# Performance work log

Measured on AMD Instinct MI355X. Metric: run time of the kernel, lower is better.

## Reference

```python
import jax, jax.numpy as jnp
import numpy as np


def _gcn_layer(h, src, dst, W, b, norm_src, norm_dst, n_nodes):
    # DGL GraphConv with norm='both': D_out^{-1/2} -> sum-aggregate -> D_in^{-1/2} -> XW + b
    m = (h * norm_src[:, None])[src]                       # [E, d] gather
    agg = jax.ops.segment_sum(m, dst, num_segments=n_nodes)  # [N, d] scatter-add
    return agg * norm_dst[:, None] @ W + b


def reference(features, src, dst, W1, b1, W2, b2):
    n_nodes = features.shape[0]
    ones = jnp.ones(src.shape[0], dtype=features.dtype)
    deg_out = jax.ops.segment_sum(ones, src, num_segments=n_nodes)
    deg_in = jax.ops.segment_sum(ones, dst, num_segments=n_nodes)
    # DGL clamps degrees to min 1 before the -1/2 power
    norm_src = jnp.clip(deg_out, 1.0, None) ** -0.5
    norm_dst = jnp.clip(deg_in, 1.0, None) ** -0.5

    h = jax.nn.relu(_gcn_layer(features, src, dst, W1, b1, norm_src, norm_dst, n_nodes))
    h = jax.nn.relu(_gcn_layer(h, src, dst, W2, b2, norm_src, norm_dst, n_nodes))
    return h


def setup_inputs() -> dict:
    key = jax.random.key(0)
    k1, k2, k3, k4, k5 = jax.random.split(key, 5)
    N, E, D = 50000, 600000, 128
    scale = 1.0 / np.sqrt(D)
    return {
        "features": jax.random.normal(k1, (N, D), dtype=jnp.float32),
        "src": jax.random.randint(k2, (E,), 0, N, dtype=jnp.int32),
        "dst": jax.random.randint(k3, (E,), 0, N, dtype=jnp.int32),
        "W1": jax.random.normal(k4, (D, D), dtype=jnp.float32) * scale,
        "b1": jnp.zeros((D,), dtype=jnp.float32),
        "W2": jax.random.normal(k5, (D, D), dtype=jnp.float32) * scale,
        "b2": jnp.zeros((D,), dtype=jnp.float32),
    }
```

## Files before the change

kernel.cpp:

```cpp
#include <hip/hip_runtime.h>

#define DIM 128
#define HBD 64
#define HBS 64
#define HWORDS 25088
#define WSTR 136

typedef __attribute__((ext_vector_type(8))) short b8;
typedef __attribute__((ext_vector_type(4))) float f4;
typedef __attribute__((ext_vector_type(8))) unsigned short u16x8;

static __device__ __forceinline__ unsigned short f2bf(float f) {
    unsigned u = __float_as_uint(f);
    u += 0x7fffu + ((u >> 16) & 1u);
    return (unsigned short)(u >> 16);
}
static __device__ __forceinline__ float bf2f(unsigned short b) {
    return __uint_as_float((unsigned)b << 16);
}

__global__ __launch_bounds__(1024) void k_hist(const int* __restrict__ src,
                                               const int* __restrict__ dst,
                                               unsigned short* __restrict__ local,
                                               unsigned* __restrict__ hist_in,
                                               unsigned* __restrict__ hist_out,
                                               int E, int W2p, int slice_d, int slice_s) {
    __shared__ unsigned h[HWORDS];
    const int t = threadIdx.x;
    const bool is_dst = blockIdx.x < HBD;
    const int b = is_dst ? blockIdx.x : blockIdx.x - HBD;
    const int slice = is_dst ? slice_d : slice_s;
    const int e0 = b * slice;
    const int e1 = min(e0 + slice, E);
    const int W4 = W2p >> 2;
    uint4* h4 = (uint4*)h;

    for (int w = t; w < W4; w += 1024) h4[w] = make_uint4(0u, 0u, 0u, 0u);
    __syncthreads();

    if (is_dst) {
        int e = e0 + t;
        int d = (e < e1) ? dst[e] : 0;
        while (e < e1) {
            int en = e + 1024;
            int dn = (en < e1) ? dst[en] : 0;
            unsigned sh = (unsigned)(d & 1) * 16u;
            unsigned old = atomicAdd(&h[d >> 1], 1u << sh);
            local[e] = (unsigned short)((old >> sh) & 0xffffu);
            e = en; d = dn;
        }
    } else {
        int e = e0 + t;
        int s = (e < e1) ? src[e] : 0;
        while (e < e1) {
            int en = e + 1024;
            int sn = (en < e1) ? src[en] : 0;
            atomicAdd(&h[s >> 1], 1u << ((unsigned)(s & 1) * 16u));
            e = en; s = sn;
        }
    }
    __syncthreads();

    uint4* o = (uint4*)((is_dst ? hist_in : hist_out) + (size_t)b * W2p);
    for (int w = t; w < W4; w += 1024) o[w] = h4[w];
}

__global__ __launch_bounds__(256) void k_colscan(unsigned* __restrict__ hist_in,
                                                 const unsigned* __restrict__ hist_out,
                                                 int* __restrict__ cnt,
                                                 int* __restrict__ deg_out,
                                                 int* __restrict__ bsum,
                                                 int W2, int W2p, int N) {
    __shared__ int wsum[4];
    int w = blockIdx.x * 256 + threadIdx.x;
    unsigned run = 0;
    if (w < W2) {
        unsigned* p = hist_in + w;
        #pragma unroll 8
        for (int b = 0; b < HBD; ++b) {
            unsigned x = *p;
            *p = run;
            run += x;
            p += W2p;
        }
        unsigned run2 = 0;
        const unsigned* q = hist_out + w;
        #pragma unroll 8
        for (int b = 0; b < HBS; ++b) { run2 += *q; q += W2p; }
        int n0 = w * 2;
        if (n0 + 1 < N) {
            *(int2*)(cnt + n0)     = make_int2((int)(run & 0xffffu), (int)(run >> 16));
            *(int2*)(deg_out + n0) = make_int2((int)(run2 & 0xffffu), (int)(run2 >> 16));
        } else {
            cnt[n0]     = (int)(run & 0xffffu);
            deg_out[n0] = (int)(run2 & 0xffffu);
            run &= 0xffffu;
        }
    }
    int tot = (int)(run & 0xffffu) + (int)(run >> 16);
    #pragma unroll
    for (int off = 32; off > 0; off >>= 1) tot += __shfl_down(tot, off, 64);
    int lane = threadIdx.x & 63, wave = threadIdx.x >> 6;
    if (lane == 0) wsum[wave] = tot;
    __syncthreads();
    if (threadIdx.x == 0)   bsum[2 * blockIdx.x]     = wsum[0] + wsum[1];
    if (threadIdx.x == 128) bsum[2 * blockIdx.x + 1] = wsum[2] + wsum[3];
}

__global__ __launch_bounds__(256) void k_edge_pass_fb(const int* __restrict__ src,
                                                      const int* __restrict__ dst,
                                                      int* __restrict__ deg_out,
                                                      int* __restrict__ cnt,
                                                      int* __restrict__ local_fb, int E) {
    int e = blockIdx.x * 256 + threadIdx.x;
    if (e < E) {
        atomicAdd(&deg_out[src[e]], 1);
        local_fb[e] = atomicAdd(&cnt[dst[e]], 1);
    }
}

__global__ __launch_bounds__(256) void k_block_reduce(const int* __restrict__ deg,
                                                      int* __restrict__ bsum, int N) {
    __shared__ int wsum[4];
    int i = blockIdx.x * 256 + threadIdx.x;
    int x = (i < N) ? deg[i] : 0;
    #pragma unroll
    for (int off = 32; off > 0; off >>= 1) x += __shfl_down(x, off, 64);
    int lane = threadIdx.x & 63, wave = threadIdx.x >> 6;
    if (lane == 0) wsum[wave] = x;
    __syncthreads();
    if (threadIdx.x == 0) bsum[blockIdx.x] = wsum[0] + wsum[1] + wsum[2] + wsum[3];
}

__global__ __launch_bounds__(256) void k_scan_final(const int* __restrict__ cnt,
                                                    const int* __restrict__ deg_out,
                                                    const int* __restrict__ bsum,
                                                    int* __restrict__ row_off,
                                                    float* __restrict__ norm_src,
                                                    float* __restrict__ norm_dst, int N) {
    __shared__ int wsum[4];
    __shared__ int base_s;
    const int t = threadIdx.x;
    const int lane = t & 63, wave = t >> 6;

    int pre = 0;
    for (int i = t; i < blockIdx.x; i += 256) pre += bsum[i];
    #pragma unroll
    for (int off = 32; off > 0; off >>= 1) pre += __shfl_down(pre, off, 64);
    if (lane == 0) wsum[wave] = pre;
    __syncthreads();
    if (t == 0) base_s = wsum[0] + wsum[1] + wsum[2] + wsum[3];
    __syncthreads();
    const int bpre_v = base_s;

    int i = blockIdx.x * 256 + t;
    int x = (i < N) ? cnt[i] : 0;
    int orig = x;
    #pragma unroll
    for (int off = 1; off < 64; off <<= 1) {
        int y = __shfl_up(x, off, 64);
        if (lane >= off) x += y;
    }
    if (lane == 63) wsum[wave] = x;
    __syncthreads();
    if (t == 0) {
        int s = 0;
        for (int w = 0; w < 4; ++w) { int tt = wsum[w]; wsum[w] = s; s += tt; }
    }
    __syncthreads();
    x += wsum[wave] + bpre_v;
    if (i < N) {
        row_off[i] = x - orig;
        int di = orig < 1 ? 1 : orig;
        norm_dst[i] = rsqrtf((float)di);
        int dov = deg_out[i]; if (dov < 1) dov = 1;
        norm_src[i] = rsqrtf((float)dov);
    }
    if (i == N - 1) row_off[N] = x;
}

__global__ __launch_bounds__(256) void k_fill_cast_prep(
        const int* __restrict__ src, const int* __restrict__ dst,
        const int* __restrict__ row_off,
        const unsigned short* __restrict__ local,
        const int* __restrict__ local_fb,
        const unsigned* __restrict__ hist_in,
        int* __restrict__ csr_src,
        const float* __restrict__ feat, const float* __restrict__ norm_src,
        unsigned short* __restrict__ fbf,
        const float* __restrict__ W1, const float* __restrict__ W2,
        unsigned short* __restrict__ w1hi, unsigned short* __restrict__ w1lo,
        unsigned short* __restrict__ w2hi, unsigned short* __restrict__ w2lo,
        int E, int W2p, int slice, int eb, int cb, int pb, int n4) {
    int bx = blockIdx.x;
    if (bx < eb) {
        int e = bx * 256 + threadIdx.x;
        if (e < E) {
            int d = dst[e];
            int pos = row_off[d];
            if (hist_in) {
                int b = e / slice;
                unsigned sh = (unsigned)(d & 1) * 16u;
                unsigned bo = (hist_in[(size_t)b * W2p + (d >> 1)] >> sh) & 0xffffu;
                pos += (int)bo + (int)local[e];
            } else {
                pos += local_fb[e];
            }
            csr_src[pos] = src[e];
        }
    } else if (bx < eb + cb) {
        int i = (bx - eb) * 256 + threadIdx.x;
        if (i < n4) {
            float4 v = ((const float4*)feat)[i];
            float ns = norm_src[i >> 5];
            ushort4 o;
            o.x = f2bf(v.x * ns); o.y = f2bf(v.y * ns);
            o.z = f2bf(v.z * ns); o.w = f2bf(v.w * ns);
            ((ushort4*)fbf)[i] = o;
        }
    } else {
        int b = bx - eb - cb;
        const float* W; unsigned short *Hi, *Lo;
        if (b < pb) { W = W1; Hi = w1hi; Lo = w1lo; } else { W = W2; Hi = w2hi; Lo = w2lo; b -= pb; }
        int e = b * 256 + threadIdx.x;
        if (e < DIM * DIM) {
            int k = e >> 7, c = e & 127;
            float w = W[e];
            unsigned short hi = f2bf(w);
            unsigned short lo = f2bf(w - bf2f(hi));
            Hi[c * DIM + k] = hi;
            Lo[c * DIM + k] = lo;
        }
    }
}

__global__ __launch_bounds__(256) void k_spmm(const unsigned short* __restrict__ hb,
                                              const int* __restrict__ csr_src,
                                              const int* __restrict__ row_off,
                                              const float* __restrict__ norm_dst,
                                              unsigned short* __restrict__ aggbf, int N) {
    int t = blockIdx.x * 256 + threadIdx.x;
    int node = t >> 4;
    int lane = t & 15;
    if (node >= N) return;
    int beg = row_off[node], end = row_off[node + 1];
    float a0[8] = {0.f, 0.f, 0.f, 0.f, 0.f, 0.f, 0.f, 0.f};
    float a1[8] = {0.f, 0.f, 0.f, 0.f, 0.f, 0.f, 0.f, 0.f};
    int i = beg;
    for (; i + 4 <= end; i += 4) {
        int s0 = csr_src[i], s1 = csr_src[i + 1], s2 = csr_src[i + 2], s3 = csr_src[i + 3];
        u16x8 u0 = *((const u16x8*)(hb + (size_t)s0 * DIM) + lane);
        u16x8 u1 = *((const u16x8*)(hb + (size_t)s1 * DIM) + lane);
        u16x8 u2 = *((const u16x8*)(hb + (size_t)s2 * DIM) + lane);
        u16x8 u3 = *((const u16x8*)(hb + (size_t)s3 * DIM) + lane);
        #pragma unroll
        for (int j = 0; j < 8; ++j) {
            a0[j] += bf2f(u0[j]);
            a1[j] += bf2f(u1[j]);
            a0[j] += bf2f(u2[j]);
            a1[j] += bf2f(u3[j]);
        }
    }
    for (; i < end; ++i) {
        int s0 = csr_src[i];
        u16x8 u0 = *((const u16x8*)(hb + (size_t)s0 * DIM) + lane);
        #pragma unroll
        for (int j = 0; j < 8; ++j) a0[j] += bf2f(u0[j]);
    }
    float nd = norm_dst[node];
    u16x8 o;
    #pragma unroll
    for (int j = 0; j < 8; ++j) o[j] = f2bf((a0[j] + a1[j]) * nd);
    *((u16x8*)(aggbf + (size_t)node * DIM) + lane) = o;
}

__global__ __launch_bounds__(256, 2) void k_gemm_mfma(
        const unsigned short* __restrict__ A,
        const unsigned short* __restrict__ Wt_hi,
        const unsigned short* __restrict__ Wt_lo,
        const float* __restrict__ bias,
        const float* __restrict__ postscale,
        float* __restrict__ outf, unsigned short* __restrict__ outbf, int N) {
    __shared__ unsigned short WH[DIM * WSTR];
    __shared__ unsigned short WL[DIM * WSTR];

    const int t = threadIdx.x;
    #pragma unroll
    for (int i = 0; i < 8; ++i) {
        int e = (t + i * 256) * 8;
        int c = e >> 7, k = e & 127;
        *(float4*)(WH + c * WSTR + k) = *(const float4*)(Wt_hi + e);
        *(float4*)(WL + c * WSTR + k) = *(const float4*)(Wt_lo + e);
    }
    __syncthreads();

    const int wv = t >> 6;
    const int l = t & 63;
    const int m = l & 15;
    const int quad = l >> 4;
    const int row_t0 = blockIdx.x * 128 + wv * 32;

    f4 acc[2][8];
    #pragma unroll
    for (int rt = 0; rt < 2; ++rt)
        #pragma unroll
        for (int ct = 0; ct < 8; ++ct)
            acc[rt][ct] = (f4){0.f, 0.f, 0.f, 0.f};

    int r0 = row_t0 + m;      if (r0 >= N) r0 = N - 1;
    int r1 = row_t0 + 16 + m; if (r1 >= N) r1 = N - 1;

    #pragma unroll
    for (int ks = 0; ks < 4; ++ks) {
        int koff = ks * 32 + quad * 8;
        b8 a0 = *(const b8*)(A + (size_t)r0 * DIM + koff);
        b8 a1 = *(const b8*)(A + (size_t)r1 * DIM + koff);
        #pragma unroll
        for (int ct = 0; ct < 8; ++ct) {
            int c = ct * 16 + m;
            b8 bh = *(const b8*)(WH + c * WSTR + koff);
            b8 bl = *(const b8*)(WL + c * WSTR + koff);
            acc[0][ct] = __builtin_amdgcn_mfma_f32_16x16x32_bf16(a0, bh, acc[0][ct], 0, 0, 0);
            acc[0][ct] = __builtin_amdgcn_mfma_f32_16x16x32_bf16(a0, bl, acc[0][ct], 0, 0, 0);
            acc[1][ct] = __builtin_amdgcn_mfma_f32_16x16x32_bf16(a1, bh, acc[1][ct], 0, 0, 0);
            acc[1][ct] = __builtin_amdgcn_mfma_f32_16x16x32_bf16(a1, bl, acc[1][ct], 0, 0, 0);
        }
    }

    #pragma unroll
    for (int rt = 0; rt < 2; ++rt) {
        int rowb = row_t0 + rt * 16 + quad * 4;
        #pragma unroll
        for (int r = 0; r < 4; ++r) {
            int gr = rowb + r;
            if (gr < N) {
                float s = postscale ? postscale[gr] : 1.f;
                #pragma unroll
                for (int ct = 0; ct < 8; ++ct) {
                    int col = ct * 16 + m;
                    float v = fmaxf(acc[rt][ct][r] + bias[col], 0.f) * s;
                    if (outbf) outbf[(size_t)gr * DIM + col] = f2bf(v);
                    else       outf[(size_t)gr * DIM + col] = v;
                }
            }
        }
    }
}

static inline size_t align_up(size_t x, size_t a) { return (x + a - 1) & ~(a - 1); }

extern "C" void kernel_launch(void* const* d_in, const int* in_sizes, int n_in,
                              void* d_out, int out_size, void* d_ws, size_t ws_size,
                              hipStream_t stream) {
    const float* features = (const float*)d_in[0];
    const int*   src      = (const int*)d_in[1];
    const int*   dst      = (const int*)d_in[2];
    const float* W1       = (const float*)d_in[3];
    const float* b1       = (const float*)d_in[4];
    const float* W2       = (const float*)d_in[5];
    const float* b2       = (const float*)d_in[6];
    float* out = (float*)d_out;

    const int N = in_sizes[0] / DIM;
    const int E = in_sizes[1];
    const int B = (N + 255) / 256;
    const int W2w = (N + 1) >> 1;
    const int W2p = (W2w + 3) & ~3;
    const int slice_d = (E + HBD - 1) / HBD;
    const int slice_s = (E + HBS - 1) / HBS;
    const int cs_blocks = (W2w + 255) / 256;

    size_t nodeb = align_up((size_t)N * 4, 256);
    char* p = (char*)d_ws;
    int*   deg_out  = (int*)p;                      p += nodeb;
    int*   cnt      = (int*)p;                      p += nodeb;
    float* norm_src = (float*)p;                    p += nodeb;
    float* norm_dst = (float*)p;                    p += nodeb;
    int*   row_off  = (int*)p;                      p += align_up((size_t)(N + 1) * 4, 256);
    int*   bsum     = (int*)p;                      p += align_up((size_t)(2 * cs_blocks) * 4, 256);
    int*   csr_src  = (int*)p;                      p += align_up((size_t)E * 4, 256);
    char*  big      = p;                            p += 2 * (size_t)N * DIM * 4;
    unsigned short* w1hi = (unsigned short*)p;      p += (size_t)DIM * DIM * 2;
    unsigned short* w1lo = (unsigned short*)p;      p += (size_t)DIM * DIM * 2;
    unsigned short* w2hi = (unsigned short*)p;      p += (size_t)DIM * DIM * 2;
    unsigned short* w2lo = (unsigned short*)p;      p += (size_t)DIM * DIM * 2;
    unsigned short* aggbf = (unsigned short*)big;
    unsigned short* h1bf  = (unsigned short*)(big + (size_t)N * DIM * 2);
    unsigned short* fbf   = (unsigned short*)(big + 3 * (size_t)N * DIM * 2);
    char* ap = big;
    unsigned short* local = (unsigned short*)ap;    ap += align_up((size_t)E * 2, 256);
    unsigned* hist_in  = (unsigned*)ap;             ap += (size_t)HBD * W2p * 4;
    unsigned* hist_out = (unsigned*)ap;             ap += (size_t)HBS * W2p * 4;
    int* local_fb = (int*)big;

    const int edge_blocks = (E + 255) / 256;
    const int spmm_blocks = (int)(((size_t)N * 16 + 255) / 256);
    const int gemm_blocks = (N + 127) / 128;
    const int n4 = N * (DIM / 4);
    const int cast_blocks = (n4 + 255) / 256;
    const int prep_blocks = (DIM * DIM + 255) / 256;
    const int fcp_blocks  = edge_blocks + cast_blocks + 2 * prep_blocks;

    const bool fast = (W2p <= HWORDS) &&
        (align_up((size_t)E * 2, 256) + (size_t)(HBD + HBS) * W2p * 4
            <= 3 * (size_t)N * DIM * 2);

    if (fast) {
        k_hist<<<HBD + HBS, 1024, 0, stream>>>(src, dst, local, hist_in, hist_out,
                                               E, W2p, slice_d, slice_s);
        k_colscan<<<cs_blocks, 256, 0, stream>>>(hist_in, hist_out, cnt, deg_out, bsum, W2w, W2p, N);
        k_scan_final<<<B, 256, 0, stream>>>(cnt, deg_out, bsum, row_off, norm_src, norm_dst, N);
        k_fill_cast_prep<<<fcp_blocks, 256, 0, stream>>>(
            src, dst, row_off, local, (const int*)nullptr, hist_in, csr_src,
            features, norm_src, fbf, W1, W2, w1hi, w1lo, w2hi, w2lo,
            E, W2p, slice_d, edge_blocks, cast_blocks, prep_blocks, n4);
    } else {
        hipMemsetAsync(deg_out, 0, nodeb * 2, stream);
        k_edge_pass_fb<<<edge_blocks, 256, 0, stream>>>(src, dst, deg_out, cnt, local_fb, E);
        k_block_reduce<<<B, 256, 0, stream>>>(cnt, bsum, N);
        k_scan_final<<<B, 256, 0, stream>>>(cnt, deg_out, bsum, row_off, norm_src, norm_dst, N);
        k_fill_cast_prep<<<fcp_blocks, 256, 0, stream>>>(
            src, dst, row_off, (const unsigned short*)nullptr, local_fb,
            (const unsigned*)nullptr, csr_src,
            features, norm_src, fbf, W1, W2, w1hi, w1lo, w2hi, w2lo,
            E, W2p, slice_d, edge_blocks, cast_blocks, prep_blocks, n4);
    }

    k_spmm<<<spmm_blocks, 256, 0, stream>>>(fbf, csr_src, row_off, norm_dst, aggbf, N);
    k_gemm_mfma<<<gemm_blocks, 256, 0, stream>>>(aggbf, w1hi, w1lo, b1, norm_src,
                                                 (float*)nullptr, h1bf, N);

    k_spmm<<<spmm_blocks, 256, 0, stream>>>(h1bf, csr_src, row_off, norm_dst, aggbf, N);
    k_gemm_mfma<<<gemm_blocks, 256, 0, stream>>>(aggbf, w2hi, w2lo, b2, (const float*)nullptr,
                                                 out, (unsigned short*)nullptr, N);
}
```

Baseline: 207.4 us.

## Fuse preprocessing launches and move source normalization into SpMM gather

```diff
diff --git a/kernel.cpp b/kernel.cpp
--- a/kernel.cpp
+++ b/kernel.cpp
@@ -24,87 +24,183 @@
                                                unsigned short* __restrict__ local,
                                                unsigned* __restrict__ hist_in,
                                                unsigned* __restrict__ hist_out,
-                                               int E, int W2p, int slice_d, int slice_s) {
-    __shared__ unsigned h[HWORDS];
+                                               const float* __restrict__ feat,
+                                               unsigned short* __restrict__ fbf,
+                                               const float* __restrict__ W1,
+                                               const float* __restrict__ W2,
+                                               unsigned short* __restrict__ w1hi,
+                                               unsigned short* __restrict__ w1lo,
+                                               unsigned short* __restrict__ w2hi,
+                                               unsigned short* __restrict__ w2lo,
+                                               int* __restrict__ scan_aux,
+                                               int E, int W2p, int slice_d, int slice_s,
+                                               int n4) {
     const int t = threadIdx.x;
-    const bool is_dst = blockIdx.x < HBD;
-    const int b = is_dst ? blockIdx.x : blockIdx.x - HBD;
-    const int slice = is_dst ? slice_d : slice_s;
-    const int e0 = b * slice;
-    const int e1 = min(e0 + slice, E);
-    const int W4 = W2p >> 2;
-    uint4* h4 = (uint4*)h;
-
-    for (int w = t; w < W4; w += 1024) h4[w] = make_uint4(0u, 0u, 0u, 0u);
-    __syncthreads();
-
-    if (is_dst) {
-        int e = e0 + t;
-        int d = (e < e1) ? dst[e] : 0;
-        while (e < e1) {
-            int en = e + 1024;
-            int dn = (en < e1) ? dst[en] : 0;
-            unsigned sh = (unsigned)(d & 1) * 16u;
-            unsigned old = atomicAdd(&h[d >> 1], 1u << sh);
-            local[e] = (unsigned short)((old >> sh) & 0xffffu);
-            e = en; d = dn;
+    const int bx = blockIdx.x;
+    if (bx < HBD + HBS) {
+        __shared__ unsigned h[HWORDS];
+        const bool is_dst = bx < HBD;
+        const int b = is_dst ? bx : bx - HBD;
+        const int slice = is_dst ? slice_d : slice_s;
+        const int e0 = b * slice;
+        const int e1 = min(e0 + slice, E);
+        const int W4 = W2p >> 2;
+        uint4* h4 = (uint4*)h;
+
+        for (int w = t; w < W4; w += 1024) h4[w] = make_uint4(0u, 0u, 0u, 0u);
+        __syncthreads();
+
+        if (is_dst) {
+            int e = e0 + t;
+            int d = (e < e1) ? dst[e] : 0;
+            while (e < e1) {
+                int en = e + 1024;
+                int dn = (en < e1) ? dst[en] : 0;
+                unsigned sh = (unsigned)(d & 1) * 16u;
+                unsigned old = atomicAdd(&h[d >> 1], 1u << sh);
+                local[e] = (unsigned short)((old >> sh) & 0xffffu);
+                e = en; d = dn;
+            }
+        } else {
+            int e = e0 + t;
+            int s = (e < e1) ? src[e] : 0;
+            while (e < e1) {
+                int en = e + 1024;
+                int sn = (en < e1) ? src[en] : 0;
+                atomicAdd(&h[s >> 1], 1u << ((unsigned)(s & 1) * 16u));
+                e = en; s = sn;
+            }
+        }
+        __syncthreads();
+
+        uint4* o = (uint4*)((is_dst ? hist_in : hist_out) + (size_t)b * W2p);
+        for (int w = t; w < W4; w += 1024) o[w] = h4[w];
+    } else if (bx < HBD + HBS + 2) {
+        int b = bx - (HBD + HBS);
+        if (b == 0 && t < 256) scan_aux[t] = 0;
+        const float* W = b ? W2 : W1;
+        unsigned short* Hi = b ? w2hi : w1hi;
+        unsigned short* Lo = b ? w2lo : w1lo;
+        for (int e = t; e < DIM * DIM; e += 1024) {
+            int k = e >> 7, c = e & 127;
+            float w = W[e];
+            unsigned short hi = f2bf(w);
+            unsigned short lo = f2bf(w - bf2f(hi));
+            Hi[c * DIM + k] = hi;
+            Lo[c * DIM + k] = lo;
         }
     } else {
-        int e = e0 + t;
-        int s = (e < e1) ? src[e] : 0;
-        while (e < e1) {
-            int en = e + 1024;
-            int sn = (en < e1) ? src[en] : 0;
-            atomicAdd(&h[s >> 1], 1u << ((unsigned)(s & 1) * 16u));
-            e = en; s = sn;
-        }
-    }
-    __syncthreads();
-
-    uint4* o = (uint4*)((is_dst ? hist_in : hist_out) + (size_t)b * W2p);
-    for (int w = t; w < W4; w += 1024) o[w] = h4[w];
-}
-
-__global__ __launch_bounds__(256) void k_colscan(unsigned* __restrict__ hist_in,
-                                                 const unsigned* __restrict__ hist_out,
-                                                 int* __restrict__ cnt,
-                                                 int* __restrict__ deg_out,
-                                                 int* __restrict__ bsum,
-                                                 int W2, int W2p, int N) {
+        int i = (bx - (HBD + HBS + 2)) * 1024 + t;
+        if (i < n4) {
+            float4 v = ((const float4*)feat)[i];
+            ushort4 o;
+            o.x = f2bf(v.x); o.y = f2bf(v.y);
+            o.z = f2bf(v.z); o.w = f2bf(v.w);
+            ((ushort4*)fbf)[i] = o;
+        }
+    }
+}
+
+__global__ __launch_bounds__(256) void k_scan(unsigned* __restrict__ hist_in,
+                                              const unsigned* __restrict__ hist_out,
+                                              int* __restrict__ partials,
+                                              int* __restrict__ flags,
+                                              int* __restrict__ row_off,
+                                              float* __restrict__ norm_src,
+                                              float* __restrict__ norm_dst,
+                                              int W2, int W2p, int N) {
     __shared__ int wsum[4];
-    int w = blockIdx.x * 256 + threadIdx.x;
-    unsigned run = 0;
+    __shared__ int wbase[4];
+    __shared__ int psum[4];
+    __shared__ int base_s;
+    const int t = threadIdx.x;
+    const int b = blockIdx.x;
+    const int w = b * 256 + t;
+    const int lane = t & 63, wave = t >> 6;
+
+    unsigned run = 0, run2 = 0;
     if (w < W2) {
         unsigned* p = hist_in + w;
         #pragma unroll 8
-        for (int b = 0; b < HBD; ++b) {
+        for (int i = 0; i < HBD; ++i) {
             unsigned x = *p;
             *p = run;
             run += x;
             p += W2p;
         }
-        unsigned run2 = 0;
         const unsigned* q = hist_out + w;
         #pragma unroll 8
-        for (int b = 0; b < HBS; ++b) { run2 += *q; q += W2p; }
-        int n0 = w * 2;
-        if (n0 + 1 < N) {
-            *(int2*)(cnt + n0)     = make_int2((int)(run & 0xffffu), (int)(run >> 16));
-            *(int2*)(deg_out + n0) = make_int2((int)(run2 & 0xffffu), (int)(run2 >> 16));
-        } else {
-            cnt[n0]     = (int)(run & 0xffffu);
-            deg_out[n0] = (int)(run2 & 0xffffu);
-            run &= 0xffffu;
-        }
-    }
-    int tot = (int)(run & 0xffffu) + (int)(run >> 16);
-    #pragma unroll
-    for (int off = 32; off > 0; off >>= 1) tot += __shfl_down(tot, off, 64);
-    int lane = threadIdx.x & 63, wave = threadIdx.x >> 6;
-    if (lane == 0) wsum[wave] = tot;
-    __syncthreads();
-    if (threadIdx.x == 0)   bsum[2 * blockIdx.x]     = wsum[0] + wsum[1];
-    if (threadIdx.x == 128) bsum[2 * blockIdx.x + 1] = wsum[2] + wsum[3];
+        for (int i = 0; i < HBS; ++i) { run2 += *q; q += W2p; }
+    }
+    const int n0 = w * 2, n1 = n0 + 1;
+    const int lo = (int)(run & 0xffffu), hi = (int)(run >> 16);
+    const int s = (w < W2) ? (lo + ((n1 < N) ? hi : 0)) : 0;
+
+    int x = s;
+    #pragma unroll
+    for (int off = 1; off < 64; off <<= 1) {
+        int y = __shfl_up(x, off, 64);
+        if (lane >= off) x += y;
+    }
+    if (lane == 63) wsum[wave] = x;
+    __syncthreads();
+    if (t == 0) {
+        int acc = 0;
+        #pragma unroll
+        for (int i = 0; i < 4; ++i) { int v = wsum[i]; wbase[i] = acc; acc += v; }
+        partials[b] = acc;
+        __threadfence();
+        atomicExch(&flags[b], 1);
+    }
+    __syncthreads();
+
+    int pre = 0;
+    if (t < b) {
+        while (atomicAdd(&flags[t], 0) == 0) { __builtin_amdgcn_s_sleep(2); }
+        pre = atomicAdd(&partials[t], 0);
+    }
+    #pragma unroll
+    for (int off = 32; off > 0; off >>= 1) pre += __shfl_down(pre, off, 64);
+    if (lane == 0) psum[wave] = pre;
+    __syncthreads();
+    if (t == 0) base_s = psum[0] + psum[1] + psum[2] + psum[3];
+    __syncthreads();
+    const int B = base_s;
+
+    if (w < W2) {
+        int tb = B + wbase[wave] + (x - s);
+        row_off[n0] = tb;
+        int dlo = lo < 1 ? 1 : lo;
+        norm_dst[n0] = rsqrtf((float)dlo);
+        int o0 = (int)(run2 & 0xffffu); if (o0 < 1) o0 = 1;
+        norm_src[n0] = rsqrtf((float)o0);
+        if (n1 < N) {
+            row_off[n1] = tb + lo;
+            int dhi = hi < 1 ? 1 : hi;
+            norm_dst[n1] = rsqrtf((float)dhi);
+            int o1 = (int)(run2 >> 16); if (o1 < 1) o1 = 1;
+            norm_src[n1] = rsqrtf((float)o1);
+            if (n1 == N - 1) row_off[N] = tb + lo + hi;
+        } else if (n0 == N - 1) {
+            row_off[N] = tb + lo;
+        }
+    }
+}
+
+__global__ __launch_bounds__(256) void k_fill(const int* __restrict__ src,
+                                              const int* __restrict__ dst,
+                                              const int* __restrict__ row_off,
+                                              const unsigned short* __restrict__ local,
+                                              const unsigned* __restrict__ hist_in,
+                                              int* __restrict__ csr_src,
+                                              int E, int W2p, int slice) {
+    int e = blockIdx.x * 256 + threadIdx.x;
+    if (e >= E) return;
+    int d = dst[e];
+    int b = e / slice;
+    unsigned sh = (unsigned)(d & 1) * 16u;
+    unsigned bo = (hist_in[(size_t)b * W2p + (d >> 1)] >> sh) & 0xffffu;
+    csr_src[row_off[d] + (int)bo + (int)local[e]] = src[e];
 }
 
 __global__ __launch_bounds__(256) void k_edge_pass_fb(const int* __restrict__ src,
@@ -179,43 +275,31 @@
     if (i == N - 1) row_off[N] = x;
 }
 
-__global__ __launch_bounds__(256) void k_fill_cast_prep(
+__global__ __launch_bounds__(256) void k_fill_cast_prep_fb(
         const int* __restrict__ src, const int* __restrict__ dst,
         const int* __restrict__ row_off,
-        const unsigned short* __restrict__ local,
         const int* __restrict__ local_fb,
-        const unsigned* __restrict__ hist_in,
         int* __restrict__ csr_src,
-        const float* __restrict__ feat, const float* __restrict__ norm_src,
+        const float* __restrict__ feat,
         unsigned short* __restrict__ fbf,
         const float* __restrict__ W1, const float* __restrict__ W2,
         unsigned short* __restrict__ w1hi, unsigned short* __restrict__ w1lo,
         unsigned short* __restrict__ w2hi, unsigned short* __restrict__ w2lo,
-        int E, int W2p, int slice, int eb, int cb, int pb, int n4) {
+        int E, int eb, int cb, int pb, int n4) {
     int bx = blockIdx.x;
     if (bx < eb) {
         int e = bx * 256 + threadIdx.x;
         if (e < E) {
             int d = dst[e];
-            int pos = row_off[d];
-            if (hist_in) {
-                int b = e / slice;
-                unsigned sh = (unsigned)(d & 1) * 16u;
-                unsigned bo = (hist_in[(size_t)b * W2p + (d >> 1)] >> sh) & 0xffffu;
-                pos += (int)bo + (int)local[e];
-            } else {
-                pos += local_fb[e];
-            }
-            csr_src[pos] = src[e];
+            csr_src[row_off[d] + local_fb[e]] = src[e];
         }
     } else if (bx < eb + cb) {
         int i = (bx - eb) * 256 + threadIdx.x;
         if (i < n4) {
             float4 v = ((const float4*)feat)[i];
-            float ns = norm_src[i >> 5];
             ushort4 o;
-            o.x = f2bf(v.x * ns); o.y = f2bf(v.y * ns);
-            o.z = f2bf(v.z * ns); o.w = f2bf(v.w * ns);
+            o.x = f2bf(v.x); o.y = f2bf(v.y);
+            o.z = f2bf(v.z); o.w = f2bf(v.w);
             ((ushort4*)fbf)[i] = o;
         }
     } else {
@@ -237,6 +321,7 @@
 __global__ __launch_bounds__(256) void k_spmm(const unsigned short* __restrict__ hb,
                                               const int* __restrict__ csr_src,
                                               const int* __restrict__ row_off,
+                                              const float* __restrict__ norm_src,
                                               const float* __restrict__ norm_dst,
                                               unsigned short* __restrict__ aggbf, int N) {
     int t = blockIdx.x * 256 + threadIdx.x;
@@ -249,23 +334,25 @@
     int i = beg;
     for (; i + 4 <= end; i += 4) {
         int s0 = csr_src[i], s1 = csr_src[i + 1], s2 = csr_src[i + 2], s3 = csr_src[i + 3];
+        float ns0 = norm_src[s0], ns1 = norm_src[s1], ns2 = norm_src[s2], ns3 = norm_src[s3];
         u16x8 u0 = *((const u16x8*)(hb + (size_t)s0 * DIM) + lane);
         u16x8 u1 = *((const u16x8*)(hb + (size_t)s1 * DIM) + lane);
         u16x8 u2 = *((const u16x8*)(hb + (size_t)s2 * DIM) + lane);
         u16x8 u3 = *((const u16x8*)(hb + (size_t)s3 * DIM) + lane);
         #pragma unroll
         for (int j = 0; j < 8; ++j) {
-            a0[j] += bf2f(u0[j]);
-            a1[j] += bf2f(u1[j]);
-            a0[j] += bf2f(u2[j]);
-            a1[j] += bf2f(u3[j]);
+            a0[j] = fmaf(bf2f(u0[j]), ns0, a0[j]);
+            a1[j] = fmaf(bf2f(u1[j]), ns1, a1[j]);
+            a0[j] = fmaf(bf2f(u2[j]), ns2, a0[j]);
+            a1[j] = fmaf(bf2f(u3[j]), ns3, a1[j]);
         }
     }
     for (; i < end; ++i) {
         int s0 = csr_src[i];
+        float ns0 = norm_src[s0];
         u16x8 u0 = *((const u16x8*)(hb + (size_t)s0 * DIM) + lane);
         #pragma unroll
-        for (int j = 0; j < 8; ++j) a0[j] += bf2f(u0[j]);
+        for (int j = 0; j < 8; ++j) a0[j] = fmaf(bf2f(u0[j]), ns0, a0[j]);
     }
     float nd = norm_dst[node];
     u16x8 o;
@@ -279,7 +366,6 @@
         const unsigned short* __restrict__ Wt_hi,
         const unsigned short* __restrict__ Wt_lo,
         const float* __restrict__ bias,
-        const float* __restrict__ postscale,
         float* __restrict__ outf, unsigned short* __restrict__ outbf, int N) {
     __shared__ unsigned short WH[DIM * WSTR];
     __shared__ unsigned short WL[DIM * WSTR];
@@ -334,11 +420,10 @@
         for (int r = 0; r < 4; ++r) {
             int gr = rowb + r;
             if (gr < N) {
-                float s = postscale ? postscale[gr] : 1.f;
                 #pragma unroll
                 for (int ct = 0; ct < 8; ++ct) {
                     int col = ct * 16 + m;
-                    float v = fmaxf(acc[rt][ct][r] + bias[col], 0.f) * s;
+                    float v = fmaxf(acc[rt][ct][r] + bias[col], 0.f);
                     if (outbf) outbf[(size_t)gr * DIM + col] = f2bf(v);
                     else       outf[(size_t)gr * DIM + col] = v;
                 }
@@ -377,7 +462,7 @@
     float* norm_src = (float*)p;                    p += nodeb;
     float* norm_dst = (float*)p;                    p += nodeb;
     int*   row_off  = (int*)p;                      p += align_up((size_t)(N + 1) * 4, 256);
-    int*   bsum     = (int*)p;                      p += align_up((size_t)(2 * cs_blocks) * 4, 256);
+    int*   scan_aux = (int*)p;                      p += align_up((size_t)(B + 256) * 4, 256);
     int*   csr_src  = (int*)p;                      p += align_up((size_t)E * 4, 256);
     char*  big      = p;                            p += 2 * (size_t)N * DIM * 4;
     unsigned short* w1hi = (unsigned short*)p;      p += (size_t)DIM * DIM * 2;
@@ -392,45 +477,48 @@
     unsigned* hist_in  = (unsigned*)ap;             ap += (size_t)HBD * W2p * 4;
     unsigned* hist_out = (unsigned*)ap;             ap += (size_t)HBS * W2p * 4;
     int* local_fb = (int*)big;
+    int* partials = scan_aux;
+    int* flags    = scan_aux + 128;
+    int* bsum     = scan_aux;
 
     const int edge_blocks = (E + 255) / 256;
     const int spmm_blocks = (int)(((size_t)N * 16 + 255) / 256);
     const int gemm_blocks = (N + 127) / 128;
     const int n4 = N * (DIM / 4);
-    const int cast_blocks = (n4 + 255) / 256;
-    const int prep_blocks = (DIM * DIM + 255) / 256;
-    const int fcp_blocks  = edge_blocks + cast_blocks + 2 * prep_blocks;
-
-    const bool fast = (W2p <= HWORDS) &&
+    const int cast_blocks1k = (n4 + 1023) / 1024;
+    const int mega_blocks = HBD + HBS + 2 + cast_blocks1k;
+
+    const bool fast = (W2p <= HWORDS) && (cs_blocks <= 256) &&
         (align_up((size_t)E * 2, 256) + (size_t)(HBD + HBS) * W2p * 4
             <= 3 * (size_t)N * DIM * 2);
 
     if (fast) {
-        k_hist<<<HBD + HBS, 1024, 0, stream>>>(src, dst, local, hist_in, hist_out,
-                                               E, W2p, slice_d, slice_s);
-        k_colscan<<<cs_blocks, 256, 0, stream>>>(hist_in, hist_out, cnt, deg_out, bsum, W2w, W2p, N);
-        k_scan_final<<<B, 256, 0, stream>>>(cnt, deg_out, bsum, row_off, norm_src, norm_dst, N);
-        k_fill_cast_prep<<<fcp_blocks, 256, 0, stream>>>(
-            src, dst, row_off, local, (const int*)nullptr, hist_in, csr_src,
-            features, norm_src, fbf, W1, W2, w1hi, w1lo, w2hi, w2lo,
-            E, W2p, slice_d, edge_blocks, cast_blocks, prep_blocks, n4);
+        k_hist<<<mega_blocks, 1024, 0, stream>>>(src, dst, local, hist_in, hist_out,
+                                                 features, fbf, W1, W2,
+                                                 w1hi, w1lo, w2hi, w2lo, scan_aux,
+                                                 E, W2p, slice_d, slice_s, n4);
+        k_scan<<<cs_blocks, 256, 0, stream>>>(hist_in, hist_out, partials, flags,
+                                              row_off, norm_src, norm_dst, W2w, W2p, N);
+        k_fill<<<edge_blocks, 256, 0, stream>>>(src, dst, row_off, local, hist_in,
+                                                csr_src, E, W2p, slice_d);
     } else {
+        const int cast_blocks = (n4 + 255) / 256;
+        const int prep_blocks = (DIM * DIM + 255) / 256;
         hipMemsetAsync(deg_out, 0, nodeb * 2, stream);
         k_edge_pass_fb<<<edge_blocks, 256, 0, stream>>>(src, dst, deg_out, cnt, local_fb, E);
         k_block_reduce<<<B, 256, 0, stream>>>(cnt, bsum, N);
         k_scan_final<<<B, 256, 0, stream>>>(cnt, deg_out, bsum, row_off, norm_src, norm_dst, N);
-        k_fill_cast_prep<<<fcp_blocks, 256, 0, stream>>>(
-            src, dst, row_off, (const unsigned short*)nullptr, local_fb,
-            (const unsigned*)nullptr, csr_src,
-            features, norm_src, fbf, W1, W2, w1hi, w1lo, w2hi, w2lo,
-            E, W2p, slice_d, edge_blocks, cast_blocks, prep_blocks, n4);
-    }
-
-    k_spmm<<<spmm_blocks, 256, 0, stream>>>(fbf, csr_src, row_off, norm_dst, aggbf, N);
-    k_gemm_mfma<<<gemm_blocks, 256, 0, stream>>>(aggbf, w1hi, w1lo, b1, norm_src,
+        k_fill_cast_prep_fb<<<edge_blocks + cast_blocks + 2 * prep_blocks, 256, 0, stream>>>(
+            src, dst, row_off, local_fb, csr_src, features, fbf,
+            W1, W2, w1hi, w1lo, w2hi, w2lo,
+            E, edge_blocks, cast_blocks, prep_blocks, n4);
+    }
+
+    k_spmm<<<spmm_blocks, 256, 0, stream>>>(fbf, csr_src, row_off, norm_src, norm_dst, aggbf, N);
+    k_gemm_mfma<<<gemm_blocks, 256, 0, stream>>>(aggbf, w1hi, w1lo, b1,
                                                  (float*)nullptr, h1bf, N);
 
-    k_spmm<<<spmm_blocks, 256, 0, stream>>>(h1bf, csr_src, row_off, norm_dst, aggbf, N);
-    k_gemm_mfma<<<gemm_blocks, 256, 0, stream>>>(aggbf, w2hi, w2lo, b2, (const float*)nullptr,
+    k_spmm<<<spmm_blocks, 256, 0, stream>>>(h1bf, csr_src, row_off, norm_src, norm_dst, aggbf, N);
+    k_gemm_mfma<<<gemm_blocks, 256, 0, stream>>>(aggbf, w2hi, w2lo, b2,
                                                  out, (unsigned short*)nullptr, N);
 }
```

Result: slower. 218.8 us (+5.5%).
